# Kernel optimization log

Measured on AMD Instinct MI355X. Metric: run time of the kernel, lower is better.

## Reference

```python
import jax, jax.numpy as jnp
import numpy as np

DIM = 1024
HEADS = 8
DH = DIM // HEADS
L_HEAD = 4   # retrieval_encoder_depth
L_TAIL = 4   # depth - retrieval_encoder_depth
MULT = 4


def setup_inputs() -> dict:
    key = jax.random.key(0)
    ks = jax.random.split(key, 10)
    w = lambda k, shape: jax.random.normal(k, shape, jnp.float32) * 0.02
    inp = {"x": jax.random.normal(ks[0], (2, 2048, DIM), jnp.float32)}
    inp["cls"] = jnp.zeros((1, 1, DIM), jnp.float32)  # nn.Parameter(torch.zeros(...))
    for i, (name, L) in enumerate((("head", L_HEAD), ("tail", L_TAIL))):
        b = ks[1 + 4 * i: 5 + 4 * i]
        inp[f"{name}_Wqkv"] = w(b[0], (L, DIM, 3 * DIM))
        inp[f"{name}_Wo"] = w(b[1], (L, DIM, DIM))
        inp[f"{name}_bo"] = jnp.zeros((L, DIM), jnp.float32)
        inp[f"{name}_W1"] = w(b[2], (L, DIM, MULT * DIM))
        inp[f"{name}_b1"] = jnp.zeros((L, MULT * DIM), jnp.float32)
        inp[f"{name}_W2"] = w(b[3], (L, MULT * DIM, DIM))
        inp[f"{name}_b2"] = jnp.zeros((L, DIM), jnp.float32)
    return inp


def _block(x, Wqkv, Wo, bo, W1, b1, W2, b2):
    b, n, d = x.shape
    scale = d ** -0.5  # NOTE: full model dim, matching the torch code
    qkv = (x @ Wqkv).reshape(b, n, 3, HEADS, DH)
    q, k, v = (jnp.moveaxis(qkv[:, :, i], 1, 2) for i in range(3))  # each [b, h, n, dh]
    dots = jnp.einsum('bhid,bhjd->bhij', q, k) * scale
    causal_mask = jnp.triu(jnp.ones((n, n), bool), 1)
    dots = jnp.where(causal_mask, -jnp.inf, dots)
    attn = jax.nn.softmax(dots, axis=-1)
    out = jnp.einsum('bhij,bhjd->bhid', attn, v)
    out = jnp.moveaxis(out, 1, 2).reshape(b, n, d)
    x = x + (out @ Wo + bo)           # Residual(Attention)
    h = jax.nn.gelu(x @ W1 + b1, approximate=False)  # torch nn.GELU is exact erf
    return x + (h @ W2 + b2)          # Residual(FeedForward)


def _stack(x, Wqkv, Wo, bo, W1, b1, W2, b2):
    for i in range(Wqkv.shape[0]):  # small fixed layer count
        x = _block(x, Wqkv[i], Wo[i], bo[i], W1[i], b1[i], W2[i], b2[i])
    return x


def reference(x, cls, head_Wqkv, head_Wo, head_bo, head_W1, head_b1, head_W2, head_b2,
              tail_Wqkv, tail_Wo, tail_bo, tail_W1, tail_b1, tail_W2, tail_b2):
    b = x.shape[0]
    cls_tok = jnp.broadcast_to(cls, (b, 1, cls.shape[-1]))
    x = jnp.concatenate([cls_tok, x], axis=1)  # [b, n+1, dim]
    x_head = _stack(x, head_Wqkv, head_Wo, head_bo, head_W1, head_b1, head_W2, head_b2)
    cls_tokens = x_head[:, 0]
    x_tail = _stack(x_head, tail_Wqkv, tail_Wo, tail_bo, tail_W1, tail_b1, tail_W2, tail_b2)
    return (x_tail, cls_tokens)
```

## Files before the change

### kernel.cpp

```cpp
#include <hip/hip_runtime.h>
#include <cstdint>
#include <cstddef>

#define SEQ   2049
#define NPAD  2176
#define BATCH 2
#define MPAD  (BATCH*NPAD)
#define NH    8
#define DH    128

typedef __attribute__((ext_vector_type(8))) short s8v;
typedef __attribute__((ext_vector_type(4))) short s4v;
typedef __attribute__((ext_vector_type(4))) float f4v;

__device__ __forceinline__ short bf16_of(float f) {
  union { float f; unsigned u; } x; x.f = f;
  unsigned r = (x.u + 0x7fffu + ((x.u >> 16) & 1u)) >> 16;
  return (short)r;
}

__device__ __forceinline__ void async_cp16(const void* g, void* l) {
  __builtin_amdgcn_global_load_lds(
      (const __attribute__((address_space(1))) unsigned*)g,
      (__attribute__((address_space(3))) unsigned*)l, 16, 0, 0);
}

__device__ __forceinline__ f4v mfma16(s8v a, s8v b, f4v c) {
  return __builtin_amdgcn_mfma_f32_16x16x32_bf16(a, b, c, 0, 0, 0);
}

__global__ void concat_cast(const float* __restrict__ x, const float* __restrict__ cls,
                            float* __restrict__ xf, short* __restrict__ xb)
{
  size_t idx = (size_t)blockIdx.x * 256 + threadIdx.x;
  size_t e = idx * 4;
  size_t rowg = e >> 10;
  int d = (int)(e & 1023);
  int b = (int)(rowg / NPAD);
  int i = (int)(rowg % NPAD);
  float4 v;
  if (i == 0)            v = *(const float4*)(cls + d);
  else if (i <= 2048)    v = *(const float4*)(x + ((size_t)b * 2048 + (i - 1)) * 1024 + d);
  else                   v = make_float4(0.f, 0.f, 0.f, 0.f);
  *(float4*)(xf + e) = v;
  const float* vp = (const float*)&v;
  s4v sb;
#pragma unroll
  for (int j = 0; j < 4; j++) sb[j] = bf16_of(vp[j]);
  *(s4v*)(xb + e) = sb;
}

__global__ void wcast_t(const float* __restrict__ W, short* __restrict__ Wt, int K, int N)
{
  __shared__ float tile[64][65];
  int n0 = blockIdx.x * 64, k0 = blockIdx.y * 64;
  int tid = threadIdx.x;
#pragma unroll
  for (int i = 0; i < 4; i++) {
    int idx = i * 256 + tid;
    int r = idx >> 4, c4 = idx & 15;
    *(float4*)&tile[r][c4 * 4] = *(const float4*)(W + (size_t)(k0 + r) * N + n0 + c4 * 4);
  }
  __syncthreads();
#pragma unroll
  for (int i = 0; i < 4; i++) {
    int idx = i * 256 + tid;
    int n = idx >> 4, k4 = idx & 15;
    s4v v;
#pragma unroll
    for (int j = 0; j < 4; j++) v[j] = bf16_of(tile[k4 * 4 + j][n]);
    *(s4v*)(Wt + (size_t)(n0 + n) * K + k0 + k4 * 4) = v;
  }
}

__global__ void v_transpose(const short* __restrict__ qkv, short* __restrict__ vT)
{
  __shared__ short tile[64][72];
  int nt = blockIdx.x;
  int hd = blockIdx.y;
  int b  = blockIdx.z;
  int h = hd >> 1, dt = hd & 1;
  int n0 = nt * 64, d0 = dt * 64;
  int tid = threadIdx.x;
#pragma unroll
  for (int i = 0; i < 16; i++) {
    int idx = i * 256 + tid;
    int r = idx >> 6, cc = idx & 63;
    tile[r][cc] = qkv[((size_t)b * NPAD + n0 + r) * 3072 + 2048 + h * 128 + d0 + cc];
  }
  __syncthreads();
#pragma unroll
  for (int i = 0; i < 16; i++) {
    int idx = i * 256 + tid;
    int r = idx >> 6, cc = idx & 63;
    vT[((size_t)(b * NH + h) * DH + d0 + r) * NPAD + n0 + cc] = tile[cc][r];
  }
}

template<int EPI>
__launch_bounds__(256, 2)
__global__ void gemm_bt(const short* __restrict__ A, const short* __restrict__ Bt,
                        const float* __restrict__ bias,
                        float* __restrict__ outf, short* __restrict__ outb,
                        int N, int K)
{
  __shared__ short As[128 * 64];
  __shared__ short Bs[128 * 64];
  const int tid = threadIdx.x;
  const int w = tid >> 6, l = tid & 63;
  const int quad = l >> 4, c = l & 15;
  const int wm = w & 1, wn = w >> 1;
  const size_t m0 = (size_t)blockIdx.y * 128;
  const size_t n0 = (size_t)blockIdx.x * 128;

  const f4v z4 = {0.f, 0.f, 0.f, 0.f};
  f4v acc[4][4];
#pragma unroll
  for (int i = 0; i < 4; i++)
#pragma unroll
    for (int j = 0; j < 4; j++) acc[i][j] = z4;

  const int ksteps = K >> 6;
  for (int ks = 0; ks < ksteps; ks++) {
    const int k0 = ks << 6;
    __syncthreads();
#pragma unroll
    for (int i = 0; i < 4; i++) {
      int chunk = (i * 4 + w) * 64 + l;
      int row = chunk >> 3, kcs = chunk & 7;
      int gkc = kcs ^ (row & 7);
      async_cp16(A  + (m0 + row) * (size_t)K + k0 + gkc * 8, As + (i * 4 + w) * 512);
      async_cp16(Bt + (n0 + row) * (size_t)K + k0 + gkc * 8, Bs + (i * 4 + w) * 512);
    }
    __syncthreads();
#pragma unroll
    for (int kk = 0; kk < 2; kk++) {
      s8v af[4], bfr[4];
      const int kc = kk * 4 + quad;
#pragma unroll
      for (int mi = 0; mi < 4; mi++) {
        int m = wm * 64 + mi * 16 + c;
        af[mi] = *(const s8v*)(As + m * 64 + ((kc ^ (m & 7)) << 3));
      }
#pragma unroll
      for (int nj = 0; nj < 4; nj++) {
        int n = wn * 64 + nj * 16 + c;
        bfr[nj] = *(const s8v*)(Bs + n * 64 + ((kc ^ (n & 7)) << 3));
      }
#pragma unroll
      for (int mi = 0; mi < 4; mi++)
#pragma unroll
        for (int nj = 0; nj < 4; nj++)
          acc[mi][nj] = mfma16(af[mi], bfr[nj], acc[mi][nj]);
    }
  }

#pragma unroll
  for (int mi = 0; mi < 4; mi++) {
#pragma unroll
    for (int nj = 0; nj < 4; nj++) {
#pragma unroll
      for (int r = 0; r < 4; r++) {
        size_t row = m0 + wm * 64 + mi * 16 + quad * 4 + r;
        size_t col = n0 + wn * 64 + nj * 16 + c;
        float v = acc[mi][nj][r];
        if (EPI >= 1) v += bias[col];
        if (EPI == 1) v = 0.5f * v * (1.f + erff(v * 0.70710678118f));
        size_t off = row * (size_t)N + col;
        if (EPI == 2) {
          float res = outf[off] + v;
          outf[off] = res;
          outb[off] = bf16_of(res);
        } else {
          outb[off] = bf16_of(v);
        }
      }
    }
  }
}

template<int EPI>
__launch_bounds__(256, 4)
__global__ void gemm_bt64(const short* __restrict__ A, const short* __restrict__ Bt,
                          const float* __restrict__ bias,
                          float* __restrict__ outf, short* __restrict__ outb,
                          int N, int K)
{
  __shared__ short As[64 * 64];
  __shared__ short Bs[128 * 64];
  const int tid = threadIdx.x;
  const int w = tid >> 6, l = tid & 63;
  const int quad = l >> 4, c = l & 15;
  const int wm = w & 1, wn = w >> 1;
  const size_t m0 = (size_t)blockIdx.y * 64;
  const size_t n0 = (size_t)blockIdx.x * 128;

  const f4v z4 = {0.f, 0.f, 0.f, 0.f};
  f4v acc[2][4];
#pragma unroll
  for (int i = 0; i < 2; i++)
#pragma unroll
    for (int j = 0; j < 4; j++) acc[i][j] = z4;

  const int ksteps = K >> 6;
  for (int ks = 0; ks < ksteps; ks++) {
    const int k0 = ks << 6;
    __syncthreads();
#pragma unroll
    for (int i = 0; i < 2; i++) {
      int chunk = (i * 4 + w) * 64 + l;
      int row = chunk >> 3, kcs = chunk & 7;
      int gkc = kcs ^ (row & 7);
      async_cp16(A + (m0 + row) * (size_t)K + k0 + gkc * 8, As + (i * 4 + w) * 512);
    }
#pragma unroll
    for (int i = 0; i < 4; i++) {
      int chunk = (i * 4 + w) * 64 + l;
      int row = chunk >> 3, kcs = chunk & 7;
      int gkc = kcs ^ (row & 7);
      async_cp16(Bt + (n0 + row) * (size_t)K + k0 + gkc * 8, Bs + (i * 4 + w) * 512);
    }
    __syncthreads();
#pragma unroll
    for (int kk = 0; kk < 2; kk++) {
      s8v af[2], bfr[4];
      const int kc = kk * 4 + quad;
#pragma unroll
      for (int mi = 0; mi < 2; mi++) {
        int m = wm * 32 + mi * 16 + c;
        af[mi] = *(const s8v*)(As + m * 64 + ((kc ^ (m & 7)) << 3));
      }
#pragma unroll
      for (int nj = 0; nj < 4; nj++) {
        int n = wn * 64 + nj * 16 + c;
        bfr[nj] = *(const s8v*)(Bs + n * 64 + ((kc ^ (n & 7)) << 3));
      }
#pragma unroll
      for (int mi = 0; mi < 2; mi++)
#pragma unroll
        for (int nj = 0; nj < 4; nj++)
          acc[mi][nj] = mfma16(af[mi], bfr[nj], acc[mi][nj]);
    }
  }

#pragma unroll
  for (int mi = 0; mi < 2; mi++) {
#pragma unroll
    for (int nj = 0; nj < 4; nj++) {
#pragma unroll
      for (int r = 0; r < 4; r++) {
        size_t row = m0 + wm * 32 + mi * 16 + quad * 4 + r;
        size_t col = n0 + wn * 64 + nj * 16 + c;
        float v = acc[mi][nj][r];
        if (EPI >= 1) v += bias[col];
        if (EPI == 1) v = 0.5f * v * (1.f + erff(v * 0.70710678118f));
        size_t off = row * (size_t)N + col;
        if (EPI == 2) {
          float res = outf[off] + v;
          outf[off] = res;
          outb[off] = bf16_of(res);
        } else {
          outb[off] = bf16_of(v);
        }
      }
    }
  }
}

__launch_bounds__(256, 3)
__global__ void flash_attn(const short* __restrict__ qkv, const short* __restrict__ vT,
                           short* __restrict__ ao)
{
  __shared__ short Ks[64 * 128];
  __shared__ short Vs[128 * 64];
  __shared__ short Ps[64 * 72];
  const int tid = threadIdx.x;
  const int w = tid >> 6, l = tid & 63;
  const int quad = l >> 4, c = l & 15;
  const int qt = 32 - blockIdx.x;
  const int h = blockIdx.y, b = blockIdx.z;
  const int q0 = qt * 64;
  const size_t qb = (size_t)b * NPAD * 3072;

  s8v qf[4];
#pragma unroll
  for (int kd = 0; kd < 4; kd++) {
    int row = q0 + w * 16 + c;
    qf[kd] = *(const s8v*)(qkv + qb + (size_t)row * 3072 + h * 128 + kd * 32 + quad * 8);
  }

  const f4v z4 = {0.f, 0.f, 0.f, 0.f};
  f4v acco[8];
#pragma unroll
  for (int dj = 0; dj < 8; dj++) acco[dj] = z4;
  float mst[4], lst[4];
#pragma unroll
  for (int r = 0; r < 4; r++) { mst[r] = -__builtin_inff(); lst[r] = 0.f; }

  const int tmaxq = (q0 + 63) >> 6;
  const int tmax = tmaxq < 32 ? tmaxq : 32;
  for (int t = 0; t <= tmax; t++) {
    const int kv0 = t << 6;
    __syncthreads();
#pragma unroll
    for (int i = 0; i < 4; i++) {
      int chunk = (i * 4 + w) * 64 + l;
      int rK = chunk >> 4, kcsK = chunk & 15;
      async_cp16(qkv + qb + (size_t)(kv0 + rK) * 3072 + 1024 + h * 128 + ((kcsK ^ (rK & 15)) * 8),
                 Ks + (i * 4 + w) * 512);
      int rV = chunk >> 3, kcsV = chunk & 7;
      async_cp16(vT + ((size_t)(b * NH + h) * DH + rV) * NPAD + kv0 + ((kcsV ^ (rV & 7)) * 8),
                 Vs + (i * 4 + w) * 512);
    }
    __syncthreads();

    f4v accs[4];
#pragma unroll
    for (int nj = 0; nj < 4; nj++) accs[nj] = z4;
#pragma unroll
    for (int kd = 0; kd < 4; kd++) {
      const int kc = kd * 4 + quad;
#pragma unroll
      for (int nj = 0; nj < 4; nj++) {
        int n = nj * 16 + c;
        s8v kf = *(const s8v*)(Ks + n * 128 + ((kc ^ (n & 15)) << 3));
        accs[nj] = mfma16(qf[kd], kf, accs[nj]);
      }
    }

    const float scale = 0.03125f;
#pragma unroll
    for (int r = 0; r < 4; r++) {
      int qg = q0 + w * 16 + quad * 4 + r;
      float s[4];
      float mx = -__builtin_inff();
#pragma unroll
      for (int nj = 0; nj < 4; nj++) {
        int kg = kv0 + nj * 16 + c;
        float v = accs[nj][r] * scale;
        v = (kg > qg || kg >= SEQ) ? -__builtin_inff() : v;
        s[nj] = v;
        mx = fmaxf(mx, v);
      }
      mx = fmaxf(mx, __shfl_xor(mx, 1));
      mx = fmaxf(mx, __shfl_xor(mx, 2));
      mx = fmaxf(mx, __shfl_xor(mx, 4));
      mx = fmaxf(mx, __shfl_xor(mx, 8));
      float mn = fmaxf(mst[r], mx);
      float a  = __expf(mst[r] - mn);
      float rs = 0.f;
#pragma unroll
      for (int nj = 0; nj < 4; nj++) {
        float p = __expf(s[nj] - mn);
        rs += p;
        Ps[(w * 16 + quad * 4 + r) * 72 + nj * 16 + c] = bf16_of(p);
      }
      rs += __shfl_xor(rs, 1);
      rs += __shfl_xor(rs, 2);
      rs += __shfl_xor(rs, 4);
      rs += __shfl_xor(rs, 8);
      mst[r] = mn;
      lst[r] = lst[r] * a + rs;
#pragma unroll
      for (int dj = 0; dj < 8; dj++) acco[dj][r] *= a;
    }

#pragma unroll
    for (int kk = 0; kk < 2; kk++) {
      s8v pf = *(const s8v*)(Ps + (w * 16 + c) * 72 + kk * 32 + quad * 8);
      const int kc = kk * 4 + quad;
#pragma unroll
      for (int dj = 0; dj < 8; dj++) {
        int n = dj * 16 + c;
        s8v vf = *(const s8v*)(Vs + n * 64 + ((kc ^ (n & 7)) << 3));
        acco[dj] = mfma16(pf, vf, acco[dj]);
      }
    }
  }

#pragma unroll
  for (int r = 0; r < 4; r++) {
    size_t row = (size_t)b * NPAD + q0 + w * 16 + quad * 4 + r;
    float inv = 1.f / lst[r];
#pragma unroll
    for (int dj = 0; dj < 8; dj++)
      ao[row * 1024 + h * 128 + dj * 16 + c] = bf16_of(acco[dj][r] * inv);
  }
}

__global__ void cls_copy(const float* __restrict__ xf, float* __restrict__ out_cls)
{
  int idx = blockIdx.x * 256 + threadIdx.x;
  int b = idx >> 10, d = idx & 1023;
  out_cls[idx] = xf[(size_t)b * NPAD * 1024 + d];
}

__global__ void final_copy(const float* __restrict__ xf, float* __restrict__ out)
{
  size_t idx = (size_t)blockIdx.x * 256 + threadIdx.x;
  size_t e = idx * 4;
  size_t r = e >> 10;
  int d = (int)(e & 1023);
  int b = (int)(r / SEQ);
  int i = (int)(r % SEQ);
  *(float4*)(out + e) = *(const float4*)(xf + ((size_t)b * NPAD + i) * 1024 + d);
}

extern "C" void kernel_launch(void* const* d_in, const int* in_sizes, int n_in,
                              void* d_out, int out_size, void* d_ws, size_t ws_size,
                              hipStream_t stream)
{
  const float* x   = (const float*)d_in[0];
  const float* cls = (const float*)d_in[1];
  const float* Wqkv_s[2] = {(const float*)d_in[2], (const float*)d_in[9]};
  const float* Wo_s[2]   = {(const float*)d_in[3], (const float*)d_in[10]};
  const float* bo_s[2]   = {(const float*)d_in[4], (const float*)d_in[11]};
  const float* W1_s[2]   = {(const float*)d_in[5], (const float*)d_in[12]};
  const float* b1_s[2]   = {(const float*)d_in[6], (const float*)d_in[13]};
  const float* W2_s[2]   = {(const float*)d_in[7], (const float*)d_in[14]};
  const float* b2_s[2]   = {(const float*)d_in[8], (const float*)d_in[15]};
  float* out = (float*)d_out;

  char* ws = (char*)d_ws;
  size_t off = 0;
  auto alloc = [&](size_t bytes) -> void* {
    void* p = ws + off;
    off += (bytes + 255) & ~(size_t)255;
    return p;
  };
  float* xf   = (float*)alloc((size_t)MPAD * 1024 * 4);
  short* xb   = (short*)alloc((size_t)MPAD * 1024 * 2);
  short* qkvb = (short*)alloc((size_t)MPAD * 3072 * 2);
  short* vT   = (short*)alloc((size_t)MPAD * 1024 * 2);
  short* aob  = (short*)alloc((size_t)MPAD * 1024 * 2);
  short* hb   = (short*)alloc((size_t)MPAD * 4096 * 2);
  short* wtq  = (short*)alloc((size_t)3072 * 1024 * 2);
  short* wto  = (short*)alloc((size_t)1024 * 1024 * 2);
  short* wt1  = (short*)alloc((size_t)4096 * 1024 * 2);
  short* wt2  = (short*)alloc((size_t)1024 * 4096 * 2);

  concat_cast<<<4352, 256, 0, stream>>>(x, cls, xf, xb);

  for (int layer = 0; layer < 8; layer++) {
    int s = layer >> 2, li = layer & 3;
    const float* Wqkv = Wqkv_s[s] + (size_t)li * 1024 * 3072;
    const float* Wo   = Wo_s[s]   + (size_t)li * 1024 * 1024;
    const float* bo   = bo_s[s]   + (size_t)li * 1024;
    const float* W1   = W1_s[s]   + (size_t)li * 1024 * 4096;
    const float* b1   = b1_s[s]   + (size_t)li * 4096;
    const float* W2   = W2_s[s]   + (size_t)li * 4096 * 1024;
    const float* b2   = b2_s[s]   + (size_t)li * 1024;

    wcast_t<<<dim3(48, 16), 256, 0, stream>>>(Wqkv, wtq, 1024, 3072);
    wcast_t<<<dim3(16, 16), 256, 0, stream>>>(Wo,   wto, 1024, 1024);
    wcast_t<<<dim3(64, 16), 256, 0, stream>>>(W1,   wt1, 1024, 4096);
    wcast_t<<<dim3(16, 64), 256, 0, stream>>>(W2,   wt2, 4096, 1024);

    gemm_bt<0><<<dim3(24, 34), 256, 0, stream>>>(xb, wtq, nullptr, nullptr, qkvb, 3072, 1024);
    v_transpose<<<dim3(34, 16, 2), 256, 0, stream>>>(qkvb, vT);
    flash_attn<<<dim3(33, 8, 2), 256, 0, stream>>>(qkvb, vT, aob);
    gemm_bt64<2><<<dim3(8, 68), 256, 0, stream>>>(aob, wto, bo, xf, xb, 1024, 1024);
    gemm_bt<1><<<dim3(32, 34), 256, 0, stream>>>(xb, wt1, b1, nullptr, hb, 4096, 1024);
    gemm_bt64<2><<<dim3(8, 68), 256, 0, stream>>>(hb, wt2, b2, xf, xb, 1024, 4096);

    if (layer == 3)
      cls_copy<<<8, 256, 0, stream>>>(xf, out + (size_t)BATCH * SEQ * 1024);
  }

  final_copy<<<4098, 256, 0, stream>>>(xf, out);
  (void)in_sizes; (void)n_in; (void)out_size; (void)ws_size;
}
```

Measured before the change: 2.750 ms.

## Double-buffer flash attention K/V tiles, transpose score MFMA, merge weight casts

Flash attention now prefetches the next K/V tile into a second LDS buffer while computing the current tile, cutting one barrier per iteration. The MFMA operands are swapped so each lane owns one query row. That turns softmax max/sum reductions into two shuffles and allows vectorized P and output stores. The four per-layer weight cast/transpose launches are merged into one kernel to cut launch overhead. The doubled LDS footprint (~73KB per block) likely limits occupancy below the requested 4 blocks per CU, possibly lower than before.

```diff
diff --git a/kernel.cpp b/kernel.cpp
--- a/kernel.cpp
+++ b/kernel.cpp
@@ -50,10 +50,21 @@
   *(s4v*)(xb + e) = sb;
 }
 
-__global__ void wcast_t(const float* __restrict__ W, short* __restrict__ Wt, int K, int N)
-{
+__global__ void wcast_all(const float* __restrict__ Wq, const float* __restrict__ Wo,
+                          const float* __restrict__ W1f, const float* __restrict__ W2f,
+                          short* __restrict__ wtq, short* __restrict__ wto,
+                          short* __restrict__ wt1, short* __restrict__ wt2)
+{
+  int bx = blockIdx.x;
+  const float* W; short* Wt; int K, N;
+  if (bx < 768)       { W = Wq;  Wt = wtq; K = 1024; N = 3072; }
+  else if (bx < 1024) { bx -= 768;  W = Wo;  Wt = wto; K = 1024; N = 1024; }
+  else if (bx < 2048) { bx -= 1024; W = W1f; Wt = wt1; K = 1024; N = 4096; }
+  else                { bx -= 2048; W = W2f; Wt = wt2; K = 4096; N = 1024; }
+  int nt = N >> 6;
+  int n0 = (bx % nt) * 64, k0 = (bx / nt) * 64;
+
   __shared__ float tile[64][65];
-  int n0 = blockIdx.x * 64, k0 = blockIdx.y * 64;
   int tid = threadIdx.x;
 #pragma unroll
   for (int i = 0; i < 4; i++) {
@@ -267,53 +278,52 @@
   }
 }
 
-__launch_bounds__(256, 3)
+__launch_bounds__(256, 4)
 __global__ void flash_attn(const short* __restrict__ qkv, const short* __restrict__ vT,
                            short* __restrict__ ao)
 {
-  __shared__ short Ks[64 * 128];
-  __shared__ short Vs[128 * 64];
-  __shared__ short Ps[64 * 72];
+  __shared__ short Ks0[64 * 128];
+  __shared__ short Ks1[64 * 128];
+  __shared__ short Vs0[128 * 64];
+  __shared__ short Vs1[128 * 64];
+  __shared__ short Pt[64 * 72];
   const int tid = threadIdx.x;
   const int w = tid >> 6, l = tid & 63;
   const int quad = l >> 4, c = l & 15;
   const int qt = 32 - blockIdx.x;
   const int h = blockIdx.y, b = blockIdx.z;
   const int q0 = qt * 64;
+  const int qg = q0 + w * 16 + c;
   const size_t qb = (size_t)b * NPAD * 3072;
+  const size_t vb = (size_t)(b * NH + h) * DH;
 
   s8v qf[4];
 #pragma unroll
-  for (int kd = 0; kd < 4; kd++) {
-    int row = q0 + w * 16 + c;
-    qf[kd] = *(const s8v*)(qkv + qb + (size_t)row * 3072 + h * 128 + kd * 32 + quad * 8);
-  }
+  for (int kd = 0; kd < 4; kd++)
+    qf[kd] = *(const s8v*)(qkv + qb + (size_t)(q0 + w * 16 + c) * 3072 + h * 128 + kd * 32 + quad * 8);
 
   const f4v z4 = {0.f, 0.f, 0.f, 0.f};
   f4v acco[8];
 #pragma unroll
   for (int dj = 0; dj < 8; dj++) acco[dj] = z4;
-  float mst[4], lst[4];
-#pragma unroll
-  for (int r = 0; r < 4; r++) { mst[r] = -__builtin_inff(); lst[r] = 0.f; }
-
-  const int tmaxq = (q0 + 63) >> 6;
-  const int tmax = tmaxq < 32 ? tmaxq : 32;
-  for (int t = 0; t <= tmax; t++) {
+  float m_run = -__builtin_inff(), l_run = 0.f;
+
+  auto do_prefetch = [&](int t, short* Ksb, short* Vsb) {
     const int kv0 = t << 6;
-    __syncthreads();
 #pragma unroll
     for (int i = 0; i < 4; i++) {
       int chunk = (i * 4 + w) * 64 + l;
       int rK = chunk >> 4, kcsK = chunk & 15;
       async_cp16(qkv + qb + (size_t)(kv0 + rK) * 3072 + 1024 + h * 128 + ((kcsK ^ (rK & 15)) * 8),
-                 Ks + (i * 4 + w) * 512);
+                 Ksb + (i * 4 + w) * 512);
       int rV = chunk >> 3, kcsV = chunk & 7;
-      async_cp16(vT + ((size_t)(b * NH + h) * DH + rV) * NPAD + kv0 + ((kcsV ^ (rV & 7)) * 8),
-                 Vs + (i * 4 + w) * 512);
-    }
-    __syncthreads();
-
+      async_cp16(vT + (vb + rV) * NPAD + kv0 + ((kcsV ^ (rV & 7)) * 8),
+                 Vsb + (i * 4 + w) * 512);
+    }
+  };
+
+  auto do_tile = [&](int t, const short* Ksb, const short* Vsb) {
+    const int kv0 = t << 6;
     f4v accs[4];
 #pragma unroll
     for (int nj = 0; nj < 4; nj++) accs[nj] = z4;
@@ -322,69 +332,87 @@
       const int kc = kd * 4 + quad;
 #pragma unroll
       for (int nj = 0; nj < 4; nj++) {
-        int n = nj * 16 + c;
-        s8v kf = *(const s8v*)(Ks + n * 128 + ((kc ^ (n & 15)) << 3));
-        accs[nj] = mfma16(qf[kd], kf, accs[nj]);
+        int m = nj * 16 + c;
+        s8v kf = *(const s8v*)(Ksb + m * 128 + ((kc ^ (m & 15)) << 3));
+        accs[nj] = mfma16(kf, qf[kd], accs[nj]);
       }
     }
 
     const float scale = 0.03125f;
-#pragma unroll
-    for (int r = 0; r < 4; r++) {
-      int qg = q0 + w * 16 + quad * 4 + r;
-      float s[4];
-      float mx = -__builtin_inff();
-#pragma unroll
-      for (int nj = 0; nj < 4; nj++) {
-        int kg = kv0 + nj * 16 + c;
+    float sv[4][4];
+    float tmx = -__builtin_inff();
+#pragma unroll
+    for (int nj = 0; nj < 4; nj++) {
+#pragma unroll
+      for (int r = 0; r < 4; r++) {
+        int kg = kv0 + nj * 16 + quad * 4 + r;
         float v = accs[nj][r] * scale;
         v = (kg > qg || kg >= SEQ) ? -__builtin_inff() : v;
-        s[nj] = v;
-        mx = fmaxf(mx, v);
-      }
-      mx = fmaxf(mx, __shfl_xor(mx, 1));
-      mx = fmaxf(mx, __shfl_xor(mx, 2));
-      mx = fmaxf(mx, __shfl_xor(mx, 4));
-      mx = fmaxf(mx, __shfl_xor(mx, 8));
-      float mn = fmaxf(mst[r], mx);
-      float a  = __expf(mst[r] - mn);
-      float rs = 0.f;
-#pragma unroll
-      for (int nj = 0; nj < 4; nj++) {
-        float p = __expf(s[nj] - mn);
+        sv[nj][r] = v;
+        tmx = fmaxf(tmx, v);
+      }
+    }
+    tmx = fmaxf(tmx, __shfl_xor(tmx, 16));
+    tmx = fmaxf(tmx, __shfl_xor(tmx, 32));
+    float mn = fmaxf(m_run, tmx);
+    float a  = __expf(m_run - mn);
+    float rs = 0.f;
+#pragma unroll
+    for (int nj = 0; nj < 4; nj++) {
+      s4v pp;
+#pragma unroll
+      for (int r = 0; r < 4; r++) {
+        float p = __expf(sv[nj][r] - mn);
         rs += p;
-        Ps[(w * 16 + quad * 4 + r) * 72 + nj * 16 + c] = bf16_of(p);
-      }
-      rs += __shfl_xor(rs, 1);
-      rs += __shfl_xor(rs, 2);
-      rs += __shfl_xor(rs, 4);
-      rs += __shfl_xor(rs, 8);
-      mst[r] = mn;
-      lst[r] = lst[r] * a + rs;
-#pragma unroll
-      for (int dj = 0; dj < 8; dj++) acco[dj][r] *= a;
-    }
+        pp[r] = bf16_of(p);
+      }
+      *(s4v*)(Pt + (w * 16 + c) * 72 + nj * 16 + quad * 4) = pp;
+    }
+    rs += __shfl_xor(rs, 16);
+    rs += __shfl_xor(rs, 32);
+    m_run = mn;
+    l_run = l_run * a + rs;
+#pragma unroll
+    for (int dj = 0; dj < 8; dj++) acco[dj] *= a;
 
 #pragma unroll
     for (int kk = 0; kk < 2; kk++) {
-      s8v pf = *(const s8v*)(Ps + (w * 16 + c) * 72 + kk * 32 + quad * 8);
+      s8v pf = *(const s8v*)(Pt + (w * 16 + c) * 72 + kk * 32 + quad * 8);
       const int kc = kk * 4 + quad;
 #pragma unroll
       for (int dj = 0; dj < 8; dj++) {
-        int n = dj * 16 + c;
-        s8v vf = *(const s8v*)(Vs + n * 64 + ((kc ^ (n & 7)) << 3));
-        acco[dj] = mfma16(pf, vf, acco[dj]);
-      }
-    }
-  }
-
-#pragma unroll
-  for (int r = 0; r < 4; r++) {
-    size_t row = (size_t)b * NPAD + q0 + w * 16 + quad * 4 + r;
-    float inv = 1.f / lst[r];
-#pragma unroll
-    for (int dj = 0; dj < 8; dj++)
-      ao[row * 1024 + h * 128 + dj * 16 + c] = bf16_of(acco[dj][r] * inv);
+        int m = dj * 16 + c;
+        s8v vf = *(const s8v*)(Vsb + m * 64 + ((kc ^ (m & 7)) << 3));
+        acco[dj] = mfma16(vf, pf, acco[dj]);
+      }
+    }
+  };
+
+  const int tmax = qt;
+  do_prefetch(0, Ks0, Vs0);
+  int t = 0;
+  for (;;) {
+    __syncthreads();
+    do_prefetch(t + 1, Ks1, Vs1);
+    do_tile(t, Ks0, Vs0);
+    if (t == tmax) break;
+    t++;
+    __syncthreads();
+    do_prefetch(t + 1, Ks0, Vs0);
+    do_tile(t, Ks1, Vs1);
+    if (t == tmax) break;
+    t++;
+  }
+  __syncthreads();
+
+  const float inv = 1.f / l_run;
+  const size_t orow = ((size_t)b * NPAD + q0 + w * 16 + c) * 1024 + h * 128;
+#pragma unroll
+  for (int dj = 0; dj < 8; dj++) {
+    s4v ov;
+#pragma unroll
+    for (int r = 0; r < 4; r++) ov[r] = bf16_of(acco[dj][r] * inv);
+    *(s4v*)(ao + orow + dj * 16 + quad * 4) = ov;
   }
 }
 
@@ -451,10 +479,7 @@
     const float* W2   = W2_s[s]   + (size_t)li * 4096 * 1024;
     const float* b2   = b2_s[s]   + (size_t)li * 1024;
 
-    wcast_t<<<dim3(48, 16), 256, 0, stream>>>(Wqkv, wtq, 1024, 3072);
-    wcast_t<<<dim3(16, 16), 256, 0, stream>>>(Wo,   wto, 1024, 1024);
-    wcast_t<<<dim3(64, 16), 256, 0, stream>>>(W1,   wt1, 1024, 4096);
-    wcast_t<<<dim3(16, 64), 256, 0, stream>>>(W2,   wt2, 4096, 1024);
+    wcast_all<<<3072, 256, 0, stream>>>(Wqkv, Wo, W1, W2, wtq, wto, wt1, wt2);
 
     gemm_bt<0><<<dim3(24, 34), 256, 0, stream>>>(xb, wtq, nullptr, nullptr, qkvb, 3072, 1024);
     v_transpose<<<dim3(34, 16, 2), 256, 0, stream>>>(qkvb, vT);
```

Result: faster. 2.515 ms (-8.5%).
